# Optimization experiments

Measured on AMD Instinct MI355X. Metric: run time of the kernel, lower is better.

## Reference

```python
import jax, jax.numpy as jnp
import numpy as np

B, Q, K, D, H, HD, HID, ED, CPB, E = 2, 300, 1024, 256, 8, 32, 32, 256, 256, 131072
N = B * Q
EPS = 1e-5


def _ln(x, g, b):
    mu = x.mean(-1, keepdims=True)
    v = ((x - mu) ** 2).mean(-1, keepdims=True)
    return (x - mu) / jnp.sqrt(v + EPS) * g + b


def setup_inputs():
    key = jax.random.key(0)
    ks = jax.random.split(key, 32)
    rn = lambda k, s, sc=0.02: jax.random.normal(k, s, jnp.float32) * sc
    return {
        "nodes": jax.random.normal(ks[0], (N, D), jnp.float32),
        "images": jax.random.normal(ks[1], (B, K, D), jnp.float32),
        "rel_coords": jax.random.normal(ks[2], (B, Q, K, 2), jnp.float32),
        "edge_feats": jax.random.normal(ks[3], (E, ED), jnp.float32),
        "edge_index": jax.random.randint(ks[4], (2, E), 0, N, jnp.int32),
        "images_mask": jnp.zeros((B, K), dtype=bool),
        "ln1_g": jnp.ones((D,)), "ln1_b": jnp.zeros((D,)),
        "ln2_g": jnp.ones((D,)), "ln2_b": jnp.zeros((D,)),
        "ln3_g": jnp.ones((D,)), "ln3_b": jnp.zeros((D,)),
        "Wni": rn(ks[5], (D, HID * H)), "bni": jnp.zeros((HID * H,)),
        "Wnj": rn(ks[6], (D, HID * H)), "bnj": jnp.zeros((HID * H,)),
        "We": rn(ks[7], (ED, HID * H)), "be": jnp.zeros((HID * H,)),
        "attn_proj": jax.random.normal(ks[8], (H, HID), jnp.float32),
        "Wmsg": rn(ks[9], (D + ED, D)), "bmsg": jnp.zeros((D,)),
        "Wg_out": rn(ks[10], (D, D)), "bg_out": jnp.zeros((D,)),
        "Wq": rn(ks[11], (D, D)), "bq": jnp.zeros((D,)),
        "Wkv": rn(ks[12], (D, 2 * D)), "bkv": jnp.zeros((2 * D,)),
        "Wc1": rn(ks[13], (2, CPB), 0.5), "bc1": jnp.zeros((CPB,)),
        "Wc2": rn(ks[14], (CPB, H), 0.1), "bc2": jnp.zeros((H,)),
        "Wc_out": rn(ks[15], (D, D)), "bc_out": jnp.zeros((D,)),
        "Wf1": rn(ks[16], (D, 4 * D)), "bf1": jnp.zeros((4 * D,)),
        "Wf2": rn(ks[17], (4 * D, D)), "bf2": jnp.zeros((D,)),
    }


def reference(nodes, images, rel_coords, edge_feats, edge_index, images_mask,
              ln1_g, ln1_b, ln2_g, ln2_b, ln3_g, ln3_b,
              Wni, bni, Wnj, bnj, We, be, attn_proj, Wmsg, bmsg, Wg_out, bg_out,
              Wq, bq, Wkv, bkv, Wc1, bc1, Wc2, bc2, Wc_out, bc_out,
              Wf1, bf1, Wf2, bf2):
    src, dst = edge_index[0], edge_index[1]
    # --- graph attention (pre-LN residual) ---
    x = _ln(nodes, ln1_g, ln1_b)
    ni, nj = x[src], x[dst]  # [E, D]
    hidden = jax.nn.leaky_relu(
        ni @ Wni + bni + nj @ Wnj + bnj + edge_feats @ We + be, 0.2)
    hidden = hidden.reshape(E, H, HID)
    logits = jnp.einsum('ehd,hd->eh', hidden, attn_proj)  # [E, H]
    m = jax.ops.segment_max(logits, src, num_segments=N)
    z = jnp.exp(logits - m[src])
    scores = z / jax.ops.segment_sum(z, src, num_segments=N)[src]  # scatter softmax
    msg = (jnp.concatenate([nj, edge_feats], -1) @ Wmsg + bmsg).reshape(E, H, HD)
    agg = jax.ops.segment_sum(msg * scores[..., None], src, num_segments=N).reshape(N, D)
    nodes = nodes + (agg @ Wg_out + bg_out)
    # --- cross attention with continuous position bias ---
    x2 = _ln(nodes, ln2_g, ln2_b).reshape(B, Q, D)
    q = (x2 @ Wq + bq).reshape(B, Q, H, HD).transpose(0, 2, 1, 3)  # [B,H,Q,hd]
    kv = (images @ Wkv + bkv).reshape(B, K, 2, H, HD)
    k = kv[:, :, 0].transpose(0, 2, 1, 3)  # [B,H,K,hd]
    v = kv[:, :, 1].transpose(0, 2, 1, 3)
    cpb = jax.nn.relu(rel_coords @ Wc1 + bc1) @ Wc2 + bc2  # [B,Q,K,H]
    bias = jnp.where(images_mask[:, None, None, :], -jnp.inf,
                     jnp.transpose(cpb, (0, 3, 1, 2)))  # [B,H,Q,K]
    att = jnp.einsum('bhqd,bhkd->bhqk', q, k) / jnp.sqrt(jnp.float32(HD)) + bias
    p = jax.nn.softmax(att, axis=-1)
    out = jnp.einsum('bhqk,bhkd->bhqd', p, v)
    out = out.reshape(B, Q, H * HD)  # faithful to original: reshape WITHOUT head transpose
    nodes = nodes + (out @ Wc_out + bc_out).reshape(N, D)
    # --- FFN (residual from the normed input, as in original) ---
    x3 = _ln(nodes, ln3_g, ln3_b)
    ff = jax.nn.gelu(x3 @ Wf1 + bf1, approximate=False) @ Wf2 + bf2
    return ff + x3
```

## Files before the change

kernel.cpp:

```cpp
#include <hip/hip_runtime.h>
#include <hip/hip_bf16.h>
#include <math.h>

#define E_   131072
#define CH_  16384
#define N_   600
#define NB_  2
#define NQ_  300
#define NK_  1024
#define NH_  8

typedef __hip_bfloat16 bf16;
typedef __bf16 bh8 __attribute__((ext_vector_type(8)));
typedef float  fx4 __attribute__((ext_vector_type(4)));

static __device__ __forceinline__ float b2f(bf16 x){ return __bfloat162float(x); }
static __device__ __forceinline__ unsigned pack2(float x, float y){
  unsigned a = __bfloat16_as_ushort(__float2bfloat16(x));
  unsigned b = __bfloat16_as_ushort(__float2bfloat16(y));
  return a | (b << 16);
}
static __device__ __forceinline__ float ldf(const void* p, size_t i, bool isf32){
  return isf32 ? ((const float*)p)[i] : b2f(((const bf16*)p)[i]);
}

constexpr int WOFF[31] = {
  0,256,512,768,1024,1280,
  1536,67072,67328,132864,
  133120,133376,
  133632,264704,
  264960,330496,330752,396288,
  396544,527616,
  528128,528640,528896,530944,
  530952,596488,
  596744,858888,859912,1122056,
  1122312};
#define NWSEG 30
#define WTOT  1122312
struct SrcTab { const void* p[NWSEG]; };

static __device__ __forceinline__ void ln_stats(float v, int t, float* r1, float* r2,
                                                float& mu, float& rstd){
  float s1 = v, s2 = v*v;
  #pragma unroll
  for (int o = 32; o; o >>= 1){ s1 += __shfl_down(s1, o); s2 += __shfl_down(s2, o); }
  if ((t & 63) == 0){ r1[t>>6] = s1; r2[t>>6] = s2; }
  __syncthreads();
  float t1 = r1[0]+r1[1]+r1[2]+r1[3];
  float t2 = r2[0]+r2[1]+r2[2]+r2[3];
  mu = t1 * (1.f/256.f);
  float var = t2 * (1.f/256.f) - mu*mu;
  rstd = rsqrtf(var + 1e-5f);
  __syncthreads();
}

__global__ void k_init(int* cnt, unsigned* mkey, float* denom,
                       const void* nodes, int* dflag){
  int i = blockIdx.x*256 + threadIdx.x;
  if (i < N_) cnt[i] = 0;
  if (i < N_*NH_){ mkey[i] = 0u; denom[i] = 0.f; }
  if (i == 0){
    const unsigned short* h = (const unsigned short*)nodes;
    int odd = 0;
    for (int j = 0; j < 64; j++){
      int e = (h[j] >> 7) & 0xFF;
      if (e < 100 || e > 150) odd++;
    }
    *dflag = (odd > 8) ? 1 : 0;
  }
}

__global__ __launch_bounds__(256) void k_cvt(SrcTab tab, float* wall, const int* dflag){
  int i = blockIdx.x*256 + threadIdx.x;
  if (i >= WTOT) return;
  bool isf32 = (*dflag != 0);
  int seg = 0;
  while (seg < NWSEG-1 && i >= WOFF[seg+1]) seg++;
  wall[i] = ldf(tab.p[seg], (size_t)(i - WOFF[seg]), isf32);
}

__global__ __launch_bounds__(256) void k_node_pre(
    const void* __restrict__ nodes, const int* __restrict__ dflag,
    const float* __restrict__ g1, const float* __restrict__ b1,
    const float* __restrict__ Wni, const float* __restrict__ Wnj, const float* __restrict__ Wmsg,
    float* __restrict__ Pni, float* __restrict__ Pnj, float* __restrict__ Pmsg)
{
  __shared__ float xs[256];
  __shared__ float r1[4], r2[4];
  int n = blockIdx.x, t = threadIdx.x;
  bool isf32 = (*dflag != 0);
  float v = ldf(nodes, (size_t)n*256 + t, isf32);
  float mu, rstd;
  ln_stats(v, t, r1, r2, mu, rstd);
  float xv = (v - mu) * rstd * g1[t] + b1[t];
  xs[t] = xv;
  __syncthreads();
  float a0 = 0.f, a1 = 0.f, a2 = 0.f;
  for (int k = 0; k < 256; k++){
    float xk = xs[k];
    a0 = fmaf(xk, Wni[k*256 + t], a0);
    a1 = fmaf(xk, Wnj[k*256 + t], a1);
    a2 = fmaf(xk, Wmsg[k*256 + t], a2);
  }
  Pni[n*256 + t] = a0; Pnj[n*256 + t] = a1; Pmsg[n*256 + t] = a2;
}

__global__ void k_prep(const void* __restrict__ We, const int* __restrict__ dflag,
                       const float* __restrict__ bni, const float* __restrict__ bnj,
                       const float* __restrict__ be,
                       bf16* __restrict__ WeT, float* __restrict__ biasH)
{
  int k = blockIdx.x, n = threadIdx.x;
  bool isf32 = (*dflag != 0);
  WeT[n*256 + k] = __float2bfloat16(ldf(We, (size_t)k*256 + n, isf32));
  if (k == 0) biasH[n] = bni[n] + bnj[n] + be[n];
}

__global__ void k_count(const int* __restrict__ ei, int* cnt){
  int e = blockIdx.x*256 + threadIdx.x;
  atomicAdd(&cnt[ei[e]], 1);
}

__global__ __launch_bounds__(1024) void k_scan(const int* __restrict__ cnt,
                                               int* offs, int* cursor){
  __shared__ int s[1024];
  int t = threadIdx.x;
  s[t] = (t < N_) ? cnt[t] : 0;
  __syncthreads();
  for (int o = 1; o < 1024; o <<= 1){
    int v = 0;
    if (t >= o) v = s[t - o];
    __syncthreads();
    if (t >= o) s[t] += v;
    __syncthreads();
  }
  if (t < N_){ int excl = (t == 0) ? 0 : s[t-1]; offs[t] = excl; cursor[t] = excl; }
  if (t == N_-1) offs[N_] = s[N_-1];
}

__global__ void k_scatter(const int* __restrict__ ei, int* cursor, int* eorder){
  int e = blockIdx.x*256 + threadIdx.x;
  int pos = atomicAdd(&cursor[ei[e]], 1);
  eorder[pos] = e;
}

__global__ __launch_bounds__(256) void k_gemm_dual(
    const void* __restrict__ A, int m_base, const int* __restrict__ dflag,
    const bf16* __restrict__ BT, bf16* __restrict__ C)
{
  __shared__ __align__(16) bf16 As[128*40];
  __shared__ __align__(16) bf16 Bs[128*40];
  int m0 = blockIdx.x * 128;
  int n0 = blockIdx.y * 128;
  int t = threadIdx.x;
  bool isf32 = (*dflag != 0);
  int wave = t >> 6, lane = t & 63;
  int wr = (wave >> 1) * 64, wc = (wave & 1) * 64;
  int lm = lane & 15, lq = lane >> 4;
  int srow = t >> 2;
  int scol = (t & 3) * 8;
  size_t r0 = (size_t)(m_base + m0 + srow) * 256;
  size_t r1 = (size_t)(m_base + m0 + 64 + srow) * 256;
  fx4 acc[4][4] = {};
  for (int kk = 0; kk < 256; kk += 32){
    uint4 pa0, pa1;
    if (isf32){
      const float* a0p = (const float*)A + r0 + kk + scol;
      const float* a1p = (const float*)A + r1 + kk + scol;
      float4 va0a = *(const float4*)(a0p);
      float4 va0b = *(const float4*)(a0p + 4);
      float4 va1a = *(const float4*)(a1p);
      float4 va1b = *(const float4*)(a1p + 4);
      pa0.x = pack2(va0a.x, va0a.y); pa0.y = pack2(va0a.z, va0a.w);
      pa0.z = pack2(va0b.x, va0b.y); pa0.w = pack2(va0b.z, va0b.w);
      pa1.x = pack2(va1a.x, va1a.y); pa1.y = pack2(va1a.z, va1a.w);
      pa1.z = pack2(va1b.x, va1b.y); pa1.w = pack2(va1b.z, va1b.w);
    } else {
      pa0 = *(const uint4*)((const bf16*)A + r0 + kk + scol);
      pa1 = *(const uint4*)((const bf16*)A + r1 + kk + scol);
    }
    float4 vb0 = *(const float4*)(BT + (size_t)(n0 + srow)      * 256 + kk + scol);
    float4 vb1 = *(const float4*)(BT + (size_t)(n0 + 64 + srow) * 256 + kk + scol);
    __syncthreads();
    *(uint4*)(As + srow*40 + scol)         = pa0;
    *(uint4*)(As + (64 + srow)*40 + scol)  = pa1;
    *(float4*)(Bs + srow*40 + scol)        = vb0;
    *(float4*)(Bs + (64 + srow)*40 + scol) = vb1;
    __syncthreads();
    bh8 af[4], bfr[4];
    #pragma unroll
    for (int mt = 0; mt < 4; mt++)
      af[mt] = *reinterpret_cast<const bh8*>(As + (wr + mt*16 + lm)*40 + lq*8);
    #pragma unroll
    for (int nt = 0; nt < 4; nt++)
      bfr[nt] = *reinterpret_cast<const bh8*>(Bs + (wc + nt*16 + lm)*40 + lq*8);
    #pragma unroll
    for (int mt = 0; mt < 4; mt++)
      #pragma unroll
      for (int nt = 0; nt < 4; nt++)
        acc[mt][nt] = __builtin_amdgcn_mfma_f32_16x16x32_bf16(af[mt], bfr[nt], acc[mt][nt], 0, 0, 0);
  }
  #pragma unroll
  for (int mt = 0; mt < 4; mt++)
    #pragma unroll
    for (int nt = 0; nt < 4; nt++)
      #pragma unroll
      for (int r = 0; r < 4; r++){
        int row = m0 + wr + mt*16 + lq*4 + r;
        int col = n0 + wc + nt*16 + lm;
        C[(size_t)row*256 + col] = __float2bfloat16(acc[mt][nt][r]);
      }
}

__global__ __launch_bounds__(256) void k_logits(
    const bf16* __restrict__ He, const float* __restrict__ Pni, const float* __restrict__ Pnj,
    const float* __restrict__ biasH, const float* __restrict__ ap, const int* __restrict__ ei,
    float* __restrict__ logits, unsigned* __restrict__ mkey, int e0chunk)
{
  __shared__ float hs[32*264];
  __shared__ int   ssh[32], dsh[32];
  __shared__ float aps[256], bhs[256];
  int t = threadIdx.x;
  int base = e0chunk + blockIdx.x*32;
  if (t < 32) ssh[t] = ei[base + t];
  else if (t < 64) dsh[t-32] = ei[E_ + base + (t - 32)];
  aps[t] = ap[t];
  bhs[t] = biasH[t];
  __syncthreads();
  int slot = (t >> 5)*33 + (t & 31);
  for (int r = 0; r < 32; r++){
    float v = b2f(He[(size_t)(base - e0chunk + r)*256 + t])
            + Pni[ssh[r]*256 + t] + Pnj[dsh[r]*256 + t] + bhs[t];
    v = (v > 0.f) ? v : 0.2f*v;
    hs[r*264 + slot] = v;
  }
  __syncthreads();
  int e = t >> 3, h = t & 7;
  const float* hr  = hs + e*264 + h*33;
  const float* apr = aps + h*32;
  float acc = 0.f;
  #pragma unroll
  for (int i = 0; i < 32; i++) acc = fmaf(hr[i], apr[i], acc);
  logits[(size_t)(base + e)*8 + h] = acc;
  unsigned ub = __float_as_uint(acc);
  unsigned key = (ub & 0x80000000u) ? ~ub : (ub | 0x80000000u);
  atomicMax(&mkey[ssh[e]*8 + h], key);
}

__global__ __launch_bounds__(256) void k_softden(
    const int* __restrict__ ei, float* __restrict__ logits,
    const unsigned* __restrict__ mkey, float* __restrict__ denom)
{
  int gid = blockIdx.x*256 + threadIdx.x;
  int e = gid >> 3, h = gid & 7;
  int s = ei[e];
  unsigned key = mkey[s*8 + h];
  unsigned ub = (key & 0x80000000u) ? (key & 0x7FFFFFFFu) : ~key;
  float m = __uint_as_float(ub);
  float a = fminf(logits[gid] - m, 0.f);
  float z = __expf(a);
  logits[gid] = z;
  atomicAdd(&denom[s*8 + h], z);
}

__global__ __launch_bounds__(256) void k_agg(
    const int* __restrict__ offs, const int* __restrict__ eorder, const int* __restrict__ ei,
    const float* __restrict__ z, const float* __restrict__ denom,
    const void* __restrict__ ef, const int* __restrict__ dflag,
    const float* __restrict__ Pmsg, const float* __restrict__ bmsg,
    const float* __restrict__ Wmsg,
    const void* __restrict__ nodes, const float* __restrict__ Wg, const float* __restrict__ bg,
    const float* __restrict__ g2, const float* __restrict__ b2v,
    const float* __restrict__ Wq, const float* __restrict__ bq,
    float* __restrict__ nodes1, float* __restrict__ qbuf)
{
  __shared__ float zsh[32*8];
  __shared__ int   esh[32];
  __shared__ int   dsh[32];
  __shared__ float sinv[8];
  __shared__ float Fs[8*257];
  __shared__ float aggs[256];
  __shared__ float r1[4], r2[4];
  int n = blockIdx.x, t = threadIdx.x;
  bool isf32 = (*dflag != 0);
  int h = t >> 5;
  int e0 = offs[n], e1 = offs[n+1];
  if (t < 8){
    float dsum = denom[n*8 + t];
    sinv[t] = (dsum > 0.f) ? 1.f/dsum : 0.f;
  }
  float facc[8] = {};
  float gacc = 0.f;
  int jz = t >> 3, hz = t & 7;
  for (int base = e0; base < e1; base += 32){
    int cnt = min(32, e1 - base);
    __syncthreads();
    if (t < cnt){ int e = eorder[base + t]; esh[t] = e; dsh[t] = ei[E_ + e]; }
    __syncthreads();
    if (jz < cnt) zsh[t] = z[(size_t)esh[jz]*8 + hz];
    __syncthreads();
    for (int jj = 0; jj < cnt; jj++){
      int e = esh[jj];
      float efv = ldf(ef, (size_t)e*256 + t, isf32);
      #pragma unroll
      for (int hq = 0; hq < 8; hq++) facc[hq] = fmaf(zsh[jj*8 + hq], efv, facc[hq]);
      gacc = fmaf(zsh[jj*8 + h], Pmsg[dsh[jj]*256 + t], gacc);
    }
  }
  __syncthreads();
  #pragma unroll
  for (int hq = 0; hq < 8; hq++) Fs[hq*257 + t] = facc[hq] * sinv[hq];
  __syncthreads();
  float am = gacc * sinv[h] + bmsg[t];
  const float* fr = Fs + h*257;
  for (int k = 0; k < 256; k++)
    am = fmaf(fr[k], Wmsg[(size_t)(256 + k)*256 + t], am);
  aggs[t] = am;
  __syncthreads();
  float o = bg[t] + ldf(nodes, (size_t)n*256 + t, isf32);
  for (int k = 0; k < 256; k++) o = fmaf(aggs[k], Wg[k*256 + t], o);
  nodes1[n*256 + t] = o;
  float mu, rstd;
  ln_stats(o, t, r1, r2, mu, rstd);
  float x2 = (o - mu) * rstd * g2[t] + b2v[t];
  __syncthreads();
  aggs[t] = x2;
  __syncthreads();
  float q = bq[t];
  for (int k = 0; k < 256; k++) q = fmaf(aggs[k], Wq[k*256 + t], q);
  qbuf[n*256 + t] = q;
}

__global__ __launch_bounds__(256) void k_kv(
    const void* __restrict__ images, const int* __restrict__ dflag,
    const float* __restrict__ Wkv, const float* __restrict__ bkv,
    float* __restrict__ kbuf, float* __restrict__ vT)
{
  __shared__ float im[256];
  int bk = blockIdx.x;
  int b = bk >> 10, ki = bk & 1023;
  int t = threadIdx.x;
  bool isf32 = (*dflag != 0);
  im[t] = ldf(images, (size_t)bk*256 + t, isf32);
  __syncthreads();
  float ko = bkv[t], vo = bkv[256 + t];
  for (int j = 0; j < 256; j++){
    float x = im[j];
    ko = fmaf(x, Wkv[j*512 + t], ko);
    vo = fmaf(x, Wkv[j*512 + 256 + t], vo);
  }
  kbuf[(size_t)bk*256 + t] = ko;
  int h = t >> 5, d = t & 31;
  vT[(((size_t)b*NH_ + h)*32 + d)*NK_ + ki] = vo;
}

__global__ __launch_bounds__(256) void k_cpb(
    const void* __restrict__ rel, const int* __restrict__ dflag,
    const float* __restrict__ Wc1, const float* __restrict__ bc1,
    const float* __restrict__ Wc2, const float* __restrict__ bc2, bf16* __restrict__ bias)
{
  __shared__ float w0[256], w1[256], bb[256], w2[256*8], b2s[8];
  int t = threadIdx.x;
  bool isf32 = (*dflag != 0);
  w0[t] = Wc1[t]; w1[t] = Wc1[256 + t]; bb[t] = bc1[t];
  for (int i = t; i < 2048; i += 256) w2[i] = Wc2[i];
  if (t < 8) b2s[t] = bc2[t];
  __syncthreads();
  size_t pos = (size_t)blockIdx.x*256 + t;
  float c0 = ldf(rel, pos*2, isf32), c1 = ldf(rel, pos*2 + 1, isf32);
  float acc[8] = {};
  for (int j = 0; j < 256; j++){
    float hj = fmaf(c0, w0[j], fmaf(c1, w1[j], bb[j]));
    hj = fmaxf(hj, 0.f);
    #pragma unroll
    for (int h = 0; h < 8; h++) acc[h] = fmaf(hj, w2[j*8 + h], acc[h]);
  }
  int k = (int)(pos & 1023);
  size_t qq = pos >> 10;
  size_t b = qq / NQ_, q = qq % NQ_;
  bf16* dst = bias + ((b*NH_)*NQ_ + q)*NK_;
  #pragma unroll
  for (int h = 0; h < 8; h++)
    dst[(size_t)h*NQ_*NK_ + k] = __float2bfloat16(acc[h] + b2s[h]);
}

__global__ __launch_bounds__(256) void k_attn(
    const float* __restrict__ qbuf, const float* __restrict__ kbuf, const float* __restrict__ vT,
    const bf16* __restrict__ bias, float* __restrict__ attn_out)
{
  __shared__ float Qs[8*33];
  __shared__ float Ks[128*33];
  __shared__ float Sc[8*1024];
  __shared__ float Op[4*8*32];
  __shared__ float qs[8];
  int qt = blockIdx.x, h = blockIdx.y, b = blockIdx.z;
  int q0 = qt*8;
  int t = threadIdx.x;
  {
    int q = t >> 5, d = t & 31;
    int gq = q0 + q;
    Qs[q*33 + d] = (gq < NQ_) ? qbuf[((size_t)b*NQ_ + gq)*256 + h*32 + d] : 0.f;
  }
  const float* kbase = kbuf + (size_t)b*NK_*256 + h*32;
  const bf16*  bb    = bias + ((size_t)(b*NH_ + h)*NQ_)*NK_;
  int kl = t & 127;
  int qb = (t >> 7) * 4;
  for (int kt = 0; kt < 8; kt++){
    int k0 = kt*128;
    __syncthreads();
    {
      int r = t >> 1, c0 = (t & 1) * 16;
      const float* src = kbase + (size_t)(k0 + r)*256 + c0;
      float* dst = Ks + r*33 + c0;
      #pragma unroll
      for (int ii = 0; ii < 4; ii++){
        float4 f = *(const float4*)(src + ii*4);
        dst[ii*4+0]=f.x; dst[ii*4+1]=f.y; dst[ii*4+2]=f.z; dst[ii*4+3]=f.w;
      }
    }
    __syncthreads();
    float a0=0.f, a1=0.f, a2=0.f, a3=0.f;
    const float* kr = Ks + kl*33;
    #pragma unroll
    for (int i = 0; i < 32; i++){
      float kd = kr[i];
      a0 = fmaf(kd, Qs[(qb+0)*33+i], a0);
      a1 = fmaf(kd, Qs[(qb+1)*33+i], a1);
      a2 = fmaf(kd, Qs[(qb+2)*33+i], a2);
      a3 = fmaf(kd, Qs[(qb+3)*33+i], a3);
    }
    float av[4] = {a0,a1,a2,a3};
    #pragma unroll
    for (int j = 0; j < 4; j++){
      int gq = min(q0 + qb + j, NQ_-1);
      float s = av[j]*0.17677669529663689f + b2f(bb[(size_t)gq*NK_ + k0 + kl]);
      Sc[(qb+j)*1024 + k0 + kl] = s;
    }
  }
  __syncthreads();
  {
    int q = t >> 5, j = t & 31;
    float m = -1e30f;
    for (int k = j; k < 1024; k += 32) m = fmaxf(m, Sc[q*1024 + k]);
    #pragma unroll
    for (int o = 16; o; o >>= 1) m = fmaxf(m, __shfl_xor(m, o));
    float ssum = 0.f;
    for (int k = j; k < 1024; k += 32){
      float e = __expf(Sc[q*1024 + k] - m);
      Sc[q*1024 + k] = e;
      ssum += e;
    }
    #pragma unroll
    for (int o = 16; o; o >>= 1) ssum += __shfl_xor(ssum, o);
    if (j == 0) qs[q] = ssum;
  }
  int d = t & 31, qg = (t >> 5) & 1, ks = t >> 6;
  const float* vrb = vT + (((size_t)(b*NH_ + h))*32)*NK_;
  float o0=0.f, o1=0.f, o2=0.f, o3=0.f;
  for (int kt = 0; kt < 8; kt++){
    int k0 = kt*128;
    __syncthreads();
    {
      int d2 = t >> 3, kq = (t & 7) * 16;
      const float* src = vrb + (size_t)d2*NK_ + k0 + kq;
      #pragma unroll
      for (int ii = 0; ii < 4; ii++){
        float4 f = *(const float4*)(src + ii*4);
        Ks[(kq+ii*4+0)*33 + d2] = f.x;
        Ks[(kq+ii*4+1)*33 + d2] = f.y;
        Ks[(kq+ii*4+2)*33 + d2] = f.z;
        Ks[(kq+ii*4+3)*33 + d2] = f.w;
      }
    }
    __syncthreads();
    const float* sc0 = Sc + (qg*4+0)*1024 + k0 + ks*32;
    const float* sc1 = Sc + (qg*4+1)*1024 + k0 + ks*32;
    const float* sc2 = Sc + (qg*4+2)*1024 + k0 + ks*32;
    const float* sc3 = Sc + (qg*4+3)*1024 + k0 + ks*32;
    #pragma unroll
    for (int kk = 0; kk < 32; kk++){
      float vv = Ks[(ks*32+kk)*33 + d];
      o0 = fmaf(sc0[kk], vv, o0);
      o1 = fmaf(sc1[kk], vv, o1);
      o2 = fmaf(sc2[kk], vv, o2);
      o3 = fmaf(sc3[kk], vv, o3);
    }
  }
  Op[((ks*8) + qg*4 + 0)*32 + d] = o0;
  Op[((ks*8) + qg*4 + 1)*32 + d] = o1;
  Op[((ks*8) + qg*4 + 2)*32 + d] = o2;
  Op[((ks*8) + qg*4 + 3)*32 + d] = o3;
  __syncthreads();
  {
    int q = t >> 5, dd = t & 31;
    int gq = q0 + q;
    if (gq < NQ_){
      float s = Op[(0*8+q)*32+dd] + Op[(1*8+q)*32+dd]
              + Op[(2*8+q)*32+dd] + Op[(3*8+q)*32+dd];
      attn_out[(((size_t)b*NH_ + h)*NQ_ + gq)*32 + dd] = s / qs[q];
    }
  }
}

__global__ __launch_bounds__(256) void k_final(
    const float* __restrict__ attn_out, const float* __restrict__ nodes1,
    const float* __restrict__ Wco, const float* __restrict__ bco,
    const float* __restrict__ g3, const float* __restrict__ b3,
    const float* __restrict__ Wf1, const float* __restrict__ bf1v,
    const float* __restrict__ Wf2, const float* __restrict__ bf2v,
    float* __restrict__ out)
{
  __shared__ float ybuf[256];
  __shared__ float x3s[256];
  __shared__ float f1s[1024];
  __shared__ float r1[4], r2[4];
  int n = blockIdx.x;
  int b = n / NQ_, qp = n % NQ_;
  int t = threadIdx.x;
  int j = t >> 5, d = t & 31;
  int tt = qp*8 + j;
  int hj = tt / NQ_, qj = tt % NQ_;
  ybuf[t] = attn_out[(((size_t)b*NH_ + hj)*NQ_ + qj)*32 + d];
  __syncthreads();
  float o = bco[t];
  for (int k = 0; k < 256; k++) o = fmaf(ybuf[k], Wco[k*256 + t], o);
  float n2 = nodes1[n*256 + t] + o;
  float mu, rstd;
  ln_stats(n2, t, r1, r2, mu, rstd);
  float x3 = (n2 - mu) * rstd * g3[t] + b3[t];
  x3s[t] = x3;
  __syncthreads();
  float a0 = bf1v[t], a1 = bf1v[256 + t], a2 = bf1v[512 + t], a3 = bf1v[768 + t];
  for (int k = 0; k < 256; k++){
    float xv = x3s[k];
    const float* wr = Wf1 + (size_t)k*1024;
    a0 = fmaf(xv, wr[t],       a0);
    a1 = fmaf(xv, wr[256 + t], a1);
    a2 = fmaf(xv, wr[512 + t], a2);
    a3 = fmaf(xv, wr[768 + t], a3);
  }
  const float c = 0.70710678118654752f;
  f1s[t]       = 0.5f*a0*(1.f + erff(a0*c));
  f1s[256 + t] = 0.5f*a1*(1.f + erff(a1*c));
  f1s[512 + t] = 0.5f*a2*(1.f + erff(a2*c));
  f1s[768 + t] = 0.5f*a3*(1.f + erff(a3*c));
  __syncthreads();
  float r = bf2v[t] + x3s[t];
  for (int k = 0; k < 1024; k++) r = fmaf(f1s[k], Wf2[(size_t)k*256 + t], r);
  out[n*256 + t] = r;
}

extern "C" void kernel_launch(void* const* d_in, const int* in_sizes, int n_in,
                              void* d_out, int out_size, void* d_ws, size_t ws_size,
                              hipStream_t stream)
{
  const void* nodes  = d_in[0];
  const void* images = d_in[1];
  const void* rel    = d_in[2];
  const void* ef     = d_in[3];
  const int*  ei     = (const int*)d_in[4];
  float* out = (float*)d_out;

  char* w = (char*)d_ws;
  auto alloc = [&](size_t bytes) -> void* {
    void* p = (void*)w; w += (bytes + 255) & ~(size_t)255; return p;
  };
  int*      dflag  = (int*)     alloc(4);
  float*    Wall   = (float*)   alloc((size_t)WTOT*4);
  bf16*     He     = (bf16*)    alloc((size_t)CH_*256*2);
  bf16*     bias   = (bf16*)    alloc((size_t)NB_*NH_*NQ_*NK_*2);
  float*    logits = (float*)   alloc((size_t)E_*8*4);
  float*    Pni    = (float*)   alloc(N_*256*4);
  float*    Pnj    = (float*)   alloc(N_*256*4);
  float*    Pmsg   = (float*)   alloc(N_*256*4);
  float*    biasH  = (float*)   alloc(256*4);
  float*    nodes1 = (float*)   alloc(N_*256*4);
  float*    qbuf   = (float*)   alloc(N_*256*4);
  float*    kbuf   = (float*)   alloc((size_t)NB_*NK_*256*4);
  float*    vT     = (float*)   alloc((size_t)NB_*NH_*32*NK_*4);
  float*    attn_o = (float*)   alloc((size_t)NB_*NH_*NQ_*32*4);
  unsigned* mkey   = (unsigned*)alloc(N_*8*4);
  float*    denom  = (float*)   alloc(N_*8*4);
  int*      cnt    = (int*)     alloc(N_*4);
  int*      offs   = (int*)     alloc((N_+1)*4);
  int*      cursor = (int*)     alloc(N_*4);
  int*      eorder = (int*)     alloc((size_t)E_*4);
  bf16*     WeT    = (bf16*)    alloc(256*256*2);

  const float *ln1g=Wall+WOFF[0],  *ln1b=Wall+WOFF[1];
  const float *ln2g=Wall+WOFF[2],  *ln2b=Wall+WOFF[3];
  const float *ln3g=Wall+WOFF[4],  *ln3b=Wall+WOFF[5];
  const float *Wni=Wall+WOFF[6],  *bni=Wall+WOFF[7];
  const float *Wnj=Wall+WOFF[8],  *bnj=Wall+WOFF[9];
  const float *be =Wall+WOFF[10], *ap =Wall+WOFF[11];
  const float *Wmsg=Wall+WOFF[12], *bmsg=Wall+WOFF[13];
  const float *Wg=Wall+WOFF[14], *bg=Wall+WOFF[15];
  const float *Wq=Wall+WOFF[16], *bq=Wall+WOFF[17];
  const float *Wkv=Wall+WOFF[18], *bkv=Wall+WOFF[19];
  const float *Wc1=Wall+WOFF[20], *bc1=Wall+WOFF[21];
  const float *Wc2=Wall+WOFF[22], *bc2=Wall+WOFF[23];
  const float *Wco=Wall+WOFF[24], *bco=Wall+WOFF[25];
  const float *Wf1=Wall+WOFF[26], *bf1v=Wall+WOFF[27];
  const float *Wf2=Wall+WOFF[28], *bf2v=Wall+WOFF[29];

  SrcTab tab;
  {
    const int idx[NWSEG] = {6,7,8,9,10,11, 12,13,14,15, 17,18, 19,20, 21,22,23,24,
                            25,26, 27,28,29,30, 31,32, 33,34,35,36};
    for (int i = 0; i < NWSEG; i++) tab.p[i] = d_in[idx[i]];
  }

  k_init    <<<19, 256, 0, stream>>>(cnt, mkey, denom, nodes, dflag);
  k_cvt     <<<(WTOT+255)/256, 256, 0, stream>>>(tab, Wall, dflag);
  k_node_pre<<<N_, 256, 0, stream>>>(nodes, dflag, ln1g, ln1b, Wni, Wnj, Wmsg, Pni, Pnj, Pmsg);
  k_prep    <<<256, 256, 0, stream>>>(d_in[16], dflag, bni, bnj, be, WeT, biasH);
  k_count   <<<E_/256, 256, 0, stream>>>(ei, cnt);
  k_scan    <<<1, 1024, 0, stream>>>(cnt, offs, cursor);
  k_scatter <<<E_/256, 256, 0, stream>>>(ei, cursor, eorder);

  dim3 ggrid(CH_/128, 2);
  for (int c = 0; c < E_/CH_; c++){
    k_gemm_dual<<<ggrid, 256, 0, stream>>>(ef, c*CH_, dflag, WeT, He);
    k_logits   <<<CH_/32, 256, 0, stream>>>(He, Pni, Pnj, biasH, ap, ei, logits, mkey, c*CH_);
  }
  k_softden <<<E_*8/256, 256, 0, stream>>>(ei, logits, mkey, denom);
  k_agg     <<<N_, 256, 0, stream>>>(offs, eorder, ei, logits, denom, ef, dflag, Pmsg, bmsg, Wmsg,
                                     nodes, Wg, bg, ln2g, ln2b, Wq, bq, nodes1, qbuf);
  k_kv      <<<NB_*NK_, 256, 0, stream>>>(images, dflag, Wkv, bkv, kbuf, vT);
  k_cpb     <<<NB_*NQ_*NK_/256, 256, 0, stream>>>(rel, dflag, Wc1, bc1, Wc2, bc2, bias);
  dim3 agrid((NQ_ + 7)/8, NH_, NB_);
  k_attn    <<<agrid, 256, 0, stream>>>(qbuf, kbuf, vT, bias, attn_o);
  k_final   <<<N_, 256, 0, stream>>>(attn_o, nodes1, Wco, bco, ln3g, ln3b,
                                     Wf1, bf1v, Wf2, bf2v, out);
}
```

Baseline: 820.4 us.

## Replace per-node scalar matvec kernels with a shared bf16 MFMA GEMM

Adds a generic 128x128-tile bf16 MFMA GEMM kernel with several epilogue modes: plain store, KV split with V transposed, bias plus residual add, and bias plus GELU to bf16. It replaces the scalar per-row FMA kernels for the node projections (Wni/Wnj/Wmsg fused into one 768-wide GEMM), the image K/V projection, the output projection and both FFN layers. A new prep kernel pre-transposes those weights to bf16. Edge aggregation is split across two blocks per node, with a separate reduce kernel, to add parallelism. The cost being removed is the repeated fp32 weight streaming per row in the old matvec kernels. In exchange, activations go through bf16 with some precision loss, and the last M tile reads rows past 600 in the A buffers.

```diff
diff --git a/kernel.cpp b/kernel.cpp
--- a/kernel.cpp
+++ b/kernel.cpp
@@ -79,41 +79,59 @@
   wall[i] = ldf(tab.p[seg], (size_t)(i - WOFF[seg]), isf32);
 }
 
-__global__ __launch_bounds__(256) void k_node_pre(
+__global__ __launch_bounds__(256) void k_prep2(
+    const void* __restrict__ WeRaw, const int* __restrict__ dflag,
+    const float* __restrict__ wall,
+    bf16* __restrict__ WeT, bf16* __restrict__ WkvT, bf16* __restrict__ WnpT,
+    bf16* __restrict__ WcoT, bf16* __restrict__ Wf1T, bf16* __restrict__ Wf2T,
+    float* __restrict__ biasH)
+{
+  int i = blockIdx.x*256 + threadIdx.x;
+  bool isf32 = (*dflag != 0);
+  const float* Wni = wall + WOFF[6];
+  const float* Wnj = wall + WOFF[8];
+  const float* Wmsg= wall + WOFF[12];
+  const float* Wkv = wall + WOFF[18];
+  const float* Wco = wall + WOFF[24];
+  const float* Wf1 = wall + WOFF[26];
+  const float* Wf2 = wall + WOFF[28];
+  if (i < 65536){
+    int n = i >> 8, k = i & 255;
+    WeT[i] = __float2bfloat16(ldf(WeRaw, (size_t)k*256 + n, isf32));
+  } else if (i < 196608){
+    int j = i - 65536; int n = j >> 8, k = j & 255;
+    WkvT[j] = __float2bfloat16(Wkv[k*512 + n]);
+  } else if (i < 393216){
+    int j = i - 196608; int n = j >> 8, k = j & 255;
+    float v = (n < 256) ? Wni[k*256 + n] : (n < 512) ? Wnj[k*256 + (n-256)]
+                        : Wmsg[k*256 + (n-512)];
+    WnpT[j] = __float2bfloat16(v);
+  } else if (i < 458752){
+    int j = i - 393216; int n = j >> 8, k = j & 255;
+    WcoT[j] = __float2bfloat16(Wco[k*256 + n]);
+  } else if (i < 720896){
+    int j = i - 458752; int n = j >> 8, k = j & 255;
+    Wf1T[j] = __float2bfloat16(Wf1[(size_t)k*1024 + n]);
+  } else if (i < 983040){
+    int j = i - 720896; int n = j >> 10, k = j & 1023;
+    Wf2T[j] = __float2bfloat16(Wf2[(size_t)k*256 + n]);
+  } else if (i < 983296){
+    int j = i - 983040;
+    biasH[j] = wall[WOFF[7]+j] + wall[WOFF[9]+j] + wall[WOFF[10]+j];
+  }
+}
+
+__global__ __launch_bounds__(256) void k_ln1(
     const void* __restrict__ nodes, const int* __restrict__ dflag,
-    const float* __restrict__ g1, const float* __restrict__ b1,
-    const float* __restrict__ Wni, const float* __restrict__ Wnj, const float* __restrict__ Wmsg,
-    float* __restrict__ Pni, float* __restrict__ Pnj, float* __restrict__ Pmsg)
-{
-  __shared__ float xs[256];
+    const float* __restrict__ g1, const float* __restrict__ b1, bf16* __restrict__ x1)
+{
   __shared__ float r1[4], r2[4];
   int n = blockIdx.x, t = threadIdx.x;
   bool isf32 = (*dflag != 0);
   float v = ldf(nodes, (size_t)n*256 + t, isf32);
   float mu, rstd;
   ln_stats(v, t, r1, r2, mu, rstd);
-  float xv = (v - mu) * rstd * g1[t] + b1[t];
-  xs[t] = xv;
-  __syncthreads();
-  float a0 = 0.f, a1 = 0.f, a2 = 0.f;
-  for (int k = 0; k < 256; k++){
-    float xk = xs[k];
-    a0 = fmaf(xk, Wni[k*256 + t], a0);
-    a1 = fmaf(xk, Wnj[k*256 + t], a1);
-    a2 = fmaf(xk, Wmsg[k*256 + t], a2);
-  }
-  Pni[n*256 + t] = a0; Pnj[n*256 + t] = a1; Pmsg[n*256 + t] = a2;
-}
-
-__global__ void k_prep(const void* __restrict__ We, const int* __restrict__ dflag,
-                       const float* __restrict__ bni, const float* __restrict__ bnj,
-                       const float* __restrict__ be,
-                       bf16* __restrict__ WeT, float* __restrict__ biasH)
-{
-  int k = blockIdx.x, n = threadIdx.x;
-  bool isf32 = (*dflag != 0);
-  WeT[n*256 + k] = __float2bfloat16(ldf(We, (size_t)k*256 + n, isf32));
-  if (k == 0) biasH[n] = bni[n] + bnj[n] + be[n];
+  x1[n*256 + t] = __float2bfloat16((v - mu) * rstd * g1[t] + b1[t]);
 }
 
 __global__ void k_count(const int* __restrict__ ei, int* cnt){
@@ -212,8 +230,100 @@
       }
 }
 
+__global__ __launch_bounds__(256) void k_gemm(
+    const void* __restrict__ A, const int* __restrict__ dflag, int adual,
+    int K, int M, const bf16* __restrict__ BT, int mode,
+    void* __restrict__ D, int ldd,
+    const float* __restrict__ bias, const float* __restrict__ add,
+    float* __restrict__ aux)
+{
+  __shared__ __align__(16) bf16 As[128*40];
+  __shared__ __align__(16) bf16 Bs[128*40];
+  int m0 = blockIdx.x * 128;
+  int n0 = blockIdx.y * 128;
+  int t = threadIdx.x;
+  bool f32src = adual && (*dflag != 0);
+  int wave = t >> 6, lane = t & 63;
+  int wr = (wave >> 1) * 64, wc = (wave & 1) * 64;
+  int lm = lane & 15, lq = lane >> 4;
+  int srow = t >> 2;
+  int scol = (t & 3) * 8;
+  size_t rA0 = (size_t)(m0 + srow) * K;
+  size_t rA1 = (size_t)(m0 + 64 + srow) * K;
+  size_t rB0 = (size_t)(n0 + srow) * K;
+  size_t rB1 = (size_t)(n0 + 64 + srow) * K;
+  fx4 acc[4][4] = {};
+  for (int kk = 0; kk < K; kk += 32){
+    uint4 pa0, pa1;
+    if (f32src){
+      const float* a0p = (const float*)A + rA0 + kk + scol;
+      const float* a1p = (const float*)A + rA1 + kk + scol;
+      float4 a = *(const float4*)(a0p), b = *(const float4*)(a0p + 4);
+      float4 c = *(const float4*)(a1p), d = *(const float4*)(a1p + 4);
+      pa0.x = pack2(a.x,a.y); pa0.y = pack2(a.z,a.w);
+      pa0.z = pack2(b.x,b.y); pa0.w = pack2(b.z,b.w);
+      pa1.x = pack2(c.x,c.y); pa1.y = pack2(c.z,c.w);
+      pa1.z = pack2(d.x,d.y); pa1.w = pack2(d.z,d.w);
+    } else {
+      pa0 = *(const uint4*)((const bf16*)A + rA0 + kk + scol);
+      pa1 = *(const uint4*)((const bf16*)A + rA1 + kk + scol);
+    }
+    float4 vb0 = *(const float4*)(BT + rB0 + kk + scol);
+    float4 vb1 = *(const float4*)(BT + rB1 + kk + scol);
+    __syncthreads();
+    *(uint4*)(As + srow*40 + scol)         = pa0;
+    *(uint4*)(As + (64 + srow)*40 + scol)  = pa1;
+    *(float4*)(Bs + srow*40 + scol)        = vb0;
+    *(float4*)(Bs + (64 + srow)*40 + scol) = vb1;
+    __syncthreads();
+    bh8 af[4], bfr[4];
+    #pragma unroll
+    for (int mt = 0; mt < 4; mt++)
+      af[mt] = *reinterpret_cast<const bh8*>(As + (wr + mt*16 + lm)*40 + lq*8);
+    #pragma unroll
+    for (int nt = 0; nt < 4; nt++)
+      bfr[nt] = *reinterpret_cast<const bh8*>(Bs + (wc + nt*16 + lm)*40 + lq*8);
+    #pragma unroll
+    for (int mt = 0; mt < 4; mt++)
+      #pragma unroll
+      for (int nt = 0; nt < 4; nt++)
+        acc[mt][nt] = __builtin_amdgcn_mfma_f32_16x16x32_bf16(af[mt], bfr[nt], acc[mt][nt], 0, 0, 0);
+  }
+  #pragma unroll
+  for (int mt = 0; mt < 4; mt++)
+    #pragma unroll
+    for (int nt = 0; nt < 4; nt++)
+      #pragma unroll
+      for (int r = 0; r < 4; r++){
+        int row = m0 + wr + mt*16 + lq*4 + r;
+        int col = n0 + wc + nt*16 + lm;
+        if (row >= M) continue;
+        float v = acc[mt][nt][r];
+        if (mode == 0){
+          if (bias) v += bias[col];
+          ((float*)D)[(size_t)row*ldd + col] = v;
+        } else if (mode == 1){
+          v += bias[col];
+          if (col < 256){
+            ((float*)D)[(size_t)row*256 + col] = v;
+          } else {
+            int b = row >> 10, ki = row & 1023;
+            int hh = (col - 256) >> 5, dd = (col - 256) & 31;
+            aux[(((size_t)b*NH_ + hh)*32 + dd)*NK_ + ki] = v;
+          }
+        } else if (mode == 2){
+          v += bias[col] + add[(size_t)row*ldd + col];
+          ((float*)D)[(size_t)row*ldd + col] = v;
+        } else {
+          v += bias[col];
+          float g = 0.5f*v*(1.f + erff(v*0.70710678118654752f));
+          ((bf16*)D)[(size_t)row*ldd + col] = __float2bfloat16(g);
+        }
+      }
+}
+
 __global__ __launch_bounds__(256) void k_logits(
-    const bf16* __restrict__ He, const float* __restrict__ Pni, const float* __restrict__ Pnj,
+    const bf16* __restrict__ He, const float* __restrict__ Pall,
     const float* __restrict__ biasH, const float* __restrict__ ap, const int* __restrict__ ei,
     float* __restrict__ logits, unsigned* __restrict__ mkey, int e0chunk)
 {
@@ -230,7 +340,7 @@
   int slot = (t >> 5)*33 + (t & 31);
   for (int r = 0; r < 32; r++){
     float v = b2f(He[(size_t)(base - e0chunk + r)*256 + t])
-            + Pni[ssh[r]*256 + t] + Pnj[dsh[r]*256 + t] + bhs[t];
+            + Pall[ssh[r]*768 + t] + Pall[dsh[r]*768 + 256 + t] + bhs[t];
     v = (v > 0.f) ? v : 0.2f*v;
     hs[r*264 + slot] = v;
   }
@@ -263,20 +373,65 @@
   atomicAdd(&denom[s*8 + h], z);
 }
 
-__global__ __launch_bounds__(256) void k_agg(
+__global__ __launch_bounds__(256) void k_agg_e(
     const int* __restrict__ offs, const int* __restrict__ eorder, const int* __restrict__ ei,
-    const float* __restrict__ z, const float* __restrict__ denom,
+    const float* __restrict__ z,
     const void* __restrict__ ef, const int* __restrict__ dflag,
-    const float* __restrict__ Pmsg, const float* __restrict__ bmsg,
-    const float* __restrict__ Wmsg,
-    const void* __restrict__ nodes, const float* __restrict__ Wg, const float* __restrict__ bg,
+    const float* __restrict__ Pall,
+    float* __restrict__ Fbuf, float* __restrict__ Gbuf)
+{
+  __shared__ float zsh[32*8];
+  __shared__ int   esh[32];
+  __shared__ int   dsh[32];
+  int n = blockIdx.x, s = blockIdx.y, t = threadIdx.x;
+  bool isf32 = (*dflag != 0);
+  int h = t >> 5;
+  int e0 = offs[n], e1 = offs[n+1];
+  int total = e1 - e0;
+  int half = (total + 1) >> 1;
+  int start = e0 + s*half;
+  int end   = min(e1, start + half);
+  float facc[8] = {};
+  float gacc = 0.f;
+  int jz = t >> 3, hz = t & 7;
+  for (int base = start; base < end; base += 32){
+    int cnt = min(32, end - base);
+    __syncthreads();
+    if (t < 32){
+      int e = (t < cnt) ? eorder[base + t] : eorder[start];
+      esh[t] = e;
+      dsh[t] = ei[E_ + e];
+    }
+    __syncthreads();
+    zsh[t] = (jz < cnt) ? z[(size_t)esh[jz]*8 + hz] : 0.f;
+    __syncthreads();
+    #pragma unroll
+    for (int jj = 0; jj < 32; jj++){
+      int e = esh[jj];
+      float efv = ldf(ef, (size_t)e*256 + t, isf32);
+      float pv  = Pall[dsh[jj]*768 + 512 + t];
+      #pragma unroll
+      for (int hq = 0; hq < 8; hq++) facc[hq] = fmaf(zsh[jj*8 + hq], efv, facc[hq]);
+      gacc = fmaf(zsh[jj*8 + h], pv, gacc);
+    }
+  }
+  int slot = n*2 + s;
+  #pragma unroll
+  for (int hq = 0; hq < 8; hq++)
+    Fbuf[((size_t)slot*8 + hq)*256 + t] = facc[hq];
+  Gbuf[(size_t)slot*256 + t] = gacc;
+}
+
+__global__ __launch_bounds__(256) void k_agg_n(
+    const float* __restrict__ Fbuf, const float* __restrict__ Gbuf,
+    const float* __restrict__ denom,
+    const float* __restrict__ bmsg, const float* __restrict__ Wmsg,
+    const void* __restrict__ nodes, const int* __restrict__ dflag,
+    const float* __restrict__ Wg, const float* __restrict__ bg,
     const float* __restrict__ g2, const float* __restrict__ b2v,
     const float* __restrict__ Wq, const float* __restrict__ bq,
     float* __restrict__ nodes1, float* __restrict__ qbuf)
 {
-  __shared__ float zsh[32*8];
-  __shared__ int   esh[32];
-  __shared__ int   dsh[32];
   __shared__ float sinv[8];
   __shared__ float Fs[8*257];
   __shared__ float aggs[256];
@@ -284,34 +439,18 @@
   int n = blockIdx.x, t = threadIdx.x;
   bool isf32 = (*dflag != 0);
   int h = t >> 5;
-  int e0 = offs[n], e1 = offs[n+1];
   if (t < 8){
     float dsum = denom[n*8 + t];
     sinv[t] = (dsum > 0.f) ? 1.f/dsum : 0.f;
   }
-  float facc[8] = {};
-  float gacc = 0.f;
-  int jz = t >> 3, hz = t & 7;
-  for (int base = e0; base < e1; base += 32){
-    int cnt = min(32, e1 - base);
-    __syncthreads();
-    if (t < cnt){ int e = eorder[base + t]; esh[t] = e; dsh[t] = ei[E_ + e]; }
-    __syncthreads();
-    if (jz < cnt) zsh[t] = z[(size_t)esh[jz]*8 + hz];
-    __syncthreads();
-    for (int jj = 0; jj < cnt; jj++){
-      int e = esh[jj];
-      float efv = ldf(ef, (size_t)e*256 + t, isf32);
-      #pragma unroll
-      for (int hq = 0; hq < 8; hq++) facc[hq] = fmaf(zsh[jj*8 + hq], efv, facc[hq]);
-      gacc = fmaf(zsh[jj*8 + h], Pmsg[dsh[jj]*256 + t], gacc);
-    }
-  }
   __syncthreads();
   #pragma unroll
-  for (int hq = 0; hq < 8; hq++) Fs[hq*257 + t] = facc[hq] * sinv[hq];
-  __syncthreads();
-  float am = gacc * sinv[h] + bmsg[t];
+  for (int hq = 0; hq < 8; hq++)
+    Fs[hq*257 + t] = (Fbuf[((size_t)(n*2)*8 + hq)*256 + t]
+                    + Fbuf[((size_t)(n*2+1)*8 + hq)*256 + t]) * sinv[hq];
+  float gacc = (Gbuf[(size_t)(n*2)*256 + t] + Gbuf[(size_t)(n*2+1)*256 + t]) * sinv[h];
+  __syncthreads();
+  float am = gacc + bmsg[t];
   const float* fr = Fs + h*257;
   for (int k = 0; k < 256; k++)
     am = fmaf(fr[k], Wmsg[(size_t)(256 + k)*256 + t], am);
@@ -329,29 +468,6 @@
   float q = bq[t];
   for (int k = 0; k < 256; k++) q = fmaf(aggs[k], Wq[k*256 + t], q);
   qbuf[n*256 + t] = q;
-}
-
-__global__ __launch_bounds__(256) void k_kv(
-    const void* __restrict__ images, const int* __restrict__ dflag,
-    const float* __restrict__ Wkv, const float* __restrict__ bkv,
-    float* __restrict__ kbuf, float* __restrict__ vT)
-{
-  __shared__ float im[256];
-  int bk = blockIdx.x;
-  int b = bk >> 10, ki = bk & 1023;
-  int t = threadIdx.x;
-  bool isf32 = (*dflag != 0);
-  im[t] = ldf(images, (size_t)bk*256 + t, isf32);
-  __syncthreads();
-  float ko = bkv[t], vo = bkv[256 + t];
-  for (int j = 0; j < 256; j++){
-    float x = im[j];
-    ko = fmaf(x, Wkv[j*512 + t], ko);
-    vo = fmaf(x, Wkv[j*512 + 256 + t], vo);
-  }
-  kbuf[(size_t)bk*256 + t] = ko;
-  int h = t >> 5, d = t & 31;
-  vT[(((size_t)b*NH_ + h)*32 + d)*NK_ + ki] = vo;
 }
 
 __global__ __launch_bounds__(256) void k_cpb(
@@ -386,7 +502,7 @@
 
 __global__ __launch_bounds__(256) void k_attn(
     const float* __restrict__ qbuf, const float* __restrict__ kbuf, const float* __restrict__ vT,
-    const bf16* __restrict__ bias, float* __restrict__ attn_out)
+    const bf16* __restrict__ bias, bf16* __restrict__ Yb)
 {
   __shared__ float Qs[8*33];
   __shared__ float Ks[128*33];
@@ -497,57 +613,25 @@
     if (gq < NQ_){
       float s = Op[(0*8+q)*32+dd] + Op[(1*8+q)*32+dd]
               + Op[(2*8+q)*32+dd] + Op[(3*8+q)*32+dd];
-      attn_out[(((size_t)b*NH_ + h)*NQ_ + gq)*32 + dd] = s / qs[q];
-    }
-  }
-}
-
-__global__ __launch_bounds__(256) void k_final(
-    const float* __restrict__ attn_out, const float* __restrict__ nodes1,
-    const float* __restrict__ Wco, const float* __restrict__ bco,
-    const float* __restrict__ g3, const float* __restrict__ b3,
-    const float* __restrict__ Wf1, const float* __restrict__ bf1v,
-    const float* __restrict__ Wf2, const float* __restrict__ bf2v,
-    float* __restrict__ out)
-{
-  __shared__ float ybuf[256];
-  __shared__ float x3s[256];
-  __shared__ float f1s[1024];
+      float sv = s / qs[q];
+      int tt = h*NQ_ + gq;
+      Yb[((size_t)b*NQ_ + (tt >> 3))*256 + (tt & 7)*32 + dd] = __float2bfloat16(sv);
+    }
+  }
+}
+
+__global__ __launch_bounds__(256) void k_ln3(
+    const float* __restrict__ n2, const float* __restrict__ g3, const float* __restrict__ b3,
+    float* __restrict__ x3f, bf16* __restrict__ x3b)
+{
   __shared__ float r1[4], r2[4];
-  int n = blockIdx.x;
-  int b = n / NQ_, qp = n % NQ_;
-  int t = threadIdx.x;
-  int j = t >> 5, d = t & 31;
-  int tt = qp*8 + j;
-  int hj = tt / NQ_, qj = tt % NQ_;
-  ybuf[t] = attn_out[(((size_t)b*NH_ + hj)*NQ_ + qj)*32 + d];
-  __syncthreads();
-  float o = bco[t];
-  for (int k = 0; k < 256; k++) o = fmaf(ybuf[k], Wco[k*256 + t], o);
-  float n2 = nodes1[n*256 + t] + o;
+  int n = blockIdx.x, t = threadIdx.x;
+  float v = n2[n*256 + t];
   float mu, rstd;
-  ln_stats(n2, t, r1, r2, mu, rstd);
-  float x3 = (n2 - mu) * rstd * g3[t] + b3[t];
-  x3s[t] = x3;
-  __syncthreads();
-  float a0 = bf1v[t], a1 = bf1v[256 + t], a2 = bf1v[512 + t], a3 = bf1v[768 + t];
-  for (int k = 0; k < 256; k++){
-    float xv = x3s[k];
-    const float* wr = Wf1 + (size_t)k*1024;
-    a0 = fmaf(xv, wr[t],       a0);
-    a1 = fmaf(xv, wr[256 + t], a1);
-    a2 = fmaf(xv, wr[512 + t], a2);
-    a3 = fmaf(xv, wr[768 + t], a3);
-  }
-  const float c = 0.70710678118654752f;
-  f1s[t]       = 0.5f*a0*(1.f + erff(a0*c));
-  f1s[256 + t] = 0.5f*a1*(1.f + erff(a1*c));
-  f1s[512 + t] = 0.5f*a2*(1.f + erff(a2*c));
-  f1s[768 + t] = 0.5f*a3*(1.f + erff(a3*c));
-  __syncthreads();
-  float r = bf2v[t] + x3s[t];
-  for (int k = 0; k < 1024; k++) r = fmaf(f1s[k], Wf2[(size_t)k*256 + t], r);
-  out[n*256 + t] = r;
+  ln_stats(v, t, r1, r2, mu, rstd);
+  float x3 = (v - mu) * rstd * g3[t] + b3[t];
+  x3f[n*256 + t] = x3;
+  x3b[n*256 + t] = __float2bfloat16(x3);
 }
 
 extern "C" void kernel_launch(void* const* d_in, const int* in_sizes, int n_in,
@@ -570,38 +654,46 @@
   bf16*     He     = (bf16*)    alloc((size_t)CH_*256*2);
   bf16*     bias   = (bf16*)    alloc((size_t)NB_*NH_*NQ_*NK_*2);
   float*    logits = (float*)   alloc((size_t)E_*8*4);
-  float*    Pni    = (float*)   alloc(N_*256*4);
-  float*    Pnj    = (float*)   alloc(N_*256*4);
-  float*    Pmsg   = (float*)   alloc(N_*256*4);
+  float*    Fbuf   = (float*)   alloc((size_t)N_*2*8*256*4);
+  float*    Gbuf   = (float*)   alloc((size_t)N_*2*256*4);
+  float*    Pall   = (float*)   alloc((size_t)N_*768*4);
   float*    biasH  = (float*)   alloc(256*4);
   float*    nodes1 = (float*)   alloc(N_*256*4);
   float*    qbuf   = (float*)   alloc(N_*256*4);
   float*    kbuf   = (float*)   alloc((size_t)NB_*NK_*256*4);
   float*    vT     = (float*)   alloc((size_t)NB_*NH_*32*NK_*4);
-  float*    attn_o = (float*)   alloc((size_t)NB_*NH_*NQ_*32*4);
+  float*    n2buf  = (float*)   alloc(N_*256*4);
+  float*    x3f    = (float*)   alloc(N_*256*4);
+  bf16*     x1     = (bf16*)    alloc(N_*256*2);
+  bf16*     x3b    = (bf16*)    alloc(N_*256*2);
+  bf16*     Yb     = (bf16*)    alloc(N_*256*2);
+  bf16*     H1     = (bf16*)    alloc((size_t)N_*1024*2);
   unsigned* mkey   = (unsigned*)alloc(N_*8*4);
   float*    denom  = (float*)   alloc(N_*8*4);
   int*      cnt    = (int*)     alloc(N_*4);
   int*      offs   = (int*)     alloc((N_+1)*4);
   int*      cursor = (int*)     alloc(N_*4);
+  bf16*     WeT    = (bf16*)    alloc(256*256*2);
+  bf16*     WkvT   = (bf16*)    alloc(512*256*2);
+  bf16*     WnpT   = (bf16*)    alloc(768*256*2);
+  bf16*     WcoT   = (bf16*)    alloc(256*256*2);
+  bf16*     Wf1T   = (bf16*)    alloc(1024*256*2);
+  bf16*     Wf2T   = (bf16*)    alloc((size_t)256*1024*2);
   int*      eorder = (int*)     alloc((size_t)E_*4);
-  bf16*     WeT    = (bf16*)    alloc(256*256*2);
 
   const float *ln1g=Wall+WOFF[0],  *ln1b=Wall+WOFF[1];
   const float *ln2g=Wall+WOFF[2],  *ln2b=Wall+WOFF[3];
   const float *ln3g=Wall+WOFF[4],  *ln3b=Wall+WOFF[5];
-  const float *Wni=Wall+WOFF[6],  *bni=Wall+WOFF[7];
-  const float *Wnj=Wall+WOFF[8],  *bnj=Wall+WOFF[9];
-  const float *be =Wall+WOFF[10], *ap =Wall+WOFF[11];
+  const float *ap =Wall+WOFF[11];
   const float *Wmsg=Wall+WOFF[12], *bmsg=Wall+WOFF[13];
   const float *Wg=Wall+WOFF[14], *bg=Wall+WOFF[15];
   const float *Wq=Wall+WOFF[16], *bq=Wall+WOFF[17];
-  const float *Wkv=Wall+WOFF[18], *bkv=Wall+WOFF[19];
+  const float *bkv=Wall+WOFF[19];
   const float *Wc1=Wall+WOFF[20], *bc1=Wall+WOFF[21];
   const float *Wc2=Wall+WOFF[22], *bc2=Wall+WOFF[23];
-  const float *Wco=Wall+WOFF[24], *bco=Wall+WOFF[25];
-  const float *Wf1=Wall+WOFF[26], *bf1v=Wall+WOFF[27];
-  const float *Wf2=Wall+WOFF[28], *bf2v=Wall+WOFF[29];
+  const float *bco=Wall+WOFF[25];
+  const float *bf1v=Wall+WOFF[27];
+  const float *bf2v=Wall+WOFF[29];
 
   SrcTab tab;
   {
@@ -610,26 +702,38 @@
     for (int i = 0; i < NWSEG; i++) tab.p[i] = d_in[idx[i]];
   }
 
-  k_init    <<<19, 256, 0, stream>>>(cnt, mkey, denom, nodes, dflag);
-  k_cvt     <<<(WTOT+255)/256, 256, 0, stream>>>(tab, Wall, dflag);
-  k_node_pre<<<N_, 256, 0, stream>>>(nodes, dflag, ln1g, ln1b, Wni, Wnj, Wmsg, Pni, Pnj, Pmsg);
-  k_prep    <<<256, 256, 0, stream>>>(d_in[16], dflag, bni, bnj, be, WeT, biasH);
-  k_count   <<<E_/256, 256, 0, stream>>>(ei, cnt);
-  k_scan    <<<1, 1024, 0, stream>>>(cnt, offs, cursor);
-  k_scatter <<<E_/256, 256, 0, stream>>>(ei, cursor, eorder);
+  k_init   <<<19, 256, 0, stream>>>(cnt, mkey, denom, nodes, dflag);
+  k_cvt    <<<(WTOT+255)/256, 256, 0, stream>>>(tab, Wall, dflag);
+  k_prep2  <<<3841, 256, 0, stream>>>(d_in[16], dflag, Wall,
+                                      WeT, WkvT, WnpT, WcoT, Wf1T, Wf2T, biasH);
+  k_ln1    <<<N_, 256, 0, stream>>>(nodes, dflag, ln1g, ln1b, x1);
+  k_count  <<<E_/256, 256, 0, stream>>>(ei, cnt);
+  k_scan   <<<1, 1024, 0, stream>>>(cnt, offs, cursor);
+  k_scatter<<<E_/256, 256, 0, stream>>>(ei, cursor, eorder);
+
+  k_gemm<<<dim3(5,6), 256, 0, stream>>>(x1, dflag, 0, 256, N_, WnpT, 0,
+                                        Pall, 768, nullptr, nullptr, nullptr);
 
   dim3 ggrid(CH_/128, 2);
   for (int c = 0; c < E_/CH_; c++){
     k_gemm_dual<<<ggrid, 256, 0, stream>>>(ef, c*CH_, dflag, WeT, He);
-    k_logits   <<<CH_/32, 256, 0, stream>>>(He, Pni, Pnj, biasH, ap, ei, logits, mkey, c*CH_);
-  }
-  k_softden <<<E_*8/256, 256, 0, stream>>>(ei, logits, mkey, denom);
-  k_agg     <<<N_, 256, 0, stream>>>(offs, eorder, ei, logits, denom, ef, dflag, Pmsg, bmsg, Wmsg,
-                                     nodes, Wg, bg, ln2g, ln2b, Wq, bq, nodes1, qbuf);
-  k_kv      <<<NB_*NK_, 256, 0, stream>>>(images, dflag, Wkv, bkv, kbuf, vT);
-  k_cpb     <<<NB_*NQ_*NK_/256, 256, 0, stream>>>(rel, dflag, Wc1, bc1, Wc2, bc2, bias);
+    k_logits   <<<CH_/32, 256, 0, stream>>>(He, Pall, biasH, ap, ei, logits, mkey, c*CH_);
+  }
+  k_softden<<<E_*8/256, 256, 0, stream>>>(ei, logits, mkey, denom);
+  k_agg_e  <<<dim3(N_,2), 256, 0, stream>>>(offs, eorder, ei, logits, ef, dflag, Pall,
+                                            Fbuf, Gbuf);
+  k_agg_n  <<<N_, 256, 0, stream>>>(Fbuf, Gbuf, denom, bmsg, Wmsg, nodes, dflag,
+                                    Wg, bg, ln2g, ln2b, Wq, bq, nodes1, qbuf);
+  k_gemm<<<dim3(16,4), 256, 0, stream>>>(images, dflag, 1, 256, NB_*NK_, WkvT, 1,
+                                         kbuf, 256, bkv, nullptr, vT);
+  k_cpb    <<<NB_*NQ_*NK_/256, 256, 0, stream>>>(rel, dflag, Wc1, bc1, Wc2, bc2, bias);
   dim3 agrid((NQ_ + 7)/8, NH_, NB_);
-  k_attn    <<<agrid, 256, 0, stream>>>(qbuf, kbuf, vT, bias, attn_o);
-  k_final   <<<N_, 256, 0, stream>>>(attn_o, nodes1, Wco, bco, ln3g, ln3b,
-                                     Wf1, bf1v, Wf2, bf2v, out);
-}
+  k_attn   <<<agrid, 256, 0, stream>>>(qbuf, kbuf, vT, bias, Yb);
+  k_gemm<<<dim3(5,2), 256, 0, stream>>>(Yb, dflag, 0, 256, N_, WcoT, 2,
+                                        n2buf, 256, bco, nodes1, nullptr);
+  k_ln3  <<<N_, 256, 0, stream>>>(n2buf, ln3g, ln3b, x3f, x3b);
+  k_gemm<<<dim3(5,8), 256, 0, stream>>>(x3b, dflag, 0, 256, N_, Wf1T, 3,
+                                        H1, 1024, bf1v, nullptr, nullptr);
+  k_gemm<<<dim3(5,2), 256, 0, stream>>>(H1, dflag, 0, 1024, N_, Wf2T, 2,
+                                        out, 256, bf2v, x3f, nullptr);
+}
```

After: 863.9 us. +5.3%, slower.
